# Optimization experiments

Measured on AMD Instinct MI355X. Metric: run time of the kernel, lower is better.

Reference implementation:

```python
import jax, jax.numpy as jnp
import numpy as np

BINS = 32
C_Z = 128
B, L = 2, 768
NUM_CLASSES = 2 * BINS + 2  # 66


def setup_inputs() -> dict:
    key = jax.random.key(0)
    k1, k2, k3 = jax.random.split(key, 3)
    residue_index = jnp.sort(jax.random.randint(k1, (B, L), 0, 1024), axis=-1)
    residue_mask = jnp.ones((B, L), dtype=bool)
    W = jax.random.normal(k2, (NUM_CLASSES, C_Z), dtype=jnp.float32)  # linear.weight.T
    b = jax.random.normal(k3, (C_Z,), dtype=jnp.float32)
    return {"residue_index": residue_index, "residue_mask": residue_mask, "W": W, "b": b}


def reference(residue_index, residue_mask, W, b):
    # pairwise relative position, clipped into bins -> class index in [1, 2*BINS+1]
    diff = residue_index[:, None, :] - residue_index[:, :, None]  # [B, L, L]
    idx = jnp.clip(diff, -BINS, BINS) + BINS + 1
    # one_hot(idx) @ W + b  ==  gather rows of W
    z = W[idx] + b  # [B, L, L, C_Z]
    pair_mask = residue_mask[:, :, None] & residue_mask[:, None, :]
    return z * pair_mask[..., None].astype(z.dtype)
```

## Files before the change

kernel.cpp:

```cpp
#include <hip/hip_runtime.h>


constexpr int BINS = 32;
constexpr int CZ   = 128;
constexpr int NC   = 2 * BINS + 2;
constexpr int B_   = 2;
constexpr int L_   = 768;
constexpr int NROWS = B_ * L_;

typedef float vfloat4 __attribute__((ext_vector_type(4)));

__global__ __launch_bounds__(256) void relpos_row_kernel(
    const int*  __restrict__ residue_index,
    const void* __restrict__ residue_mask,
    const float* __restrict__ W,
    const float* __restrict__ bias,
    float* __restrict__ out)
{
    __shared__ float wb[NC * CZ];
    __shared__ int   ridx_row[L_];
    __shared__ float mask_row[L_];

    const int tid = threadIdx.x;
    const int row = blockIdx.x;
    const int b   = row / L_;
    const int i   = row - b * L_;
    const int o   = b * L_;

    const unsigned int v0 = *(const unsigned int*)residue_mask;
    const bool byte_layout = (v0 & 0xFFFFFF00u) != 0u;

    const vfloat4* W4  = (const vfloat4*)W;
    const vfloat4* bi4 = (const vfloat4*)bias;
    vfloat4* wb4 = (vfloat4*)wb;
    for (int k = tid; k < NC * CZ / 4; k += 256) {
        wb4[k] = W4[k] + bi4[k & (CZ / 4 - 1)];
    }
    for (int k = tid; k < L_; k += 256) {
        ridx_row[k] = residue_index[o + k];
        int m = byte_layout ? (int)((const unsigned char*)residue_mask)[o + k]
                            : ((const int*)residue_mask)[o + k];
        mask_row[k] = m ? 1.0f : 0.0f;
    }
    __syncthreads();

    const int   ri_i = ridx_row[i];
    const float m_i  = mask_row[i];

    const int group = tid >> 5;
    const int lane  = tid & 31;
    float* rowout = out + (size_t)row * L_ * CZ;

    #pragma unroll 4
    for (int j = group; j < L_; j += 8) {
        const int diff = ridx_row[j] - ri_i;
        const int idx  = min(max(diff, -BINS), BINS) + BINS + 1;
        const float m  = m_i * mask_row[j];

        vfloat4 v = ((const vfloat4*)(wb + idx * CZ))[lane];
        v *= m;
        ((vfloat4*)(rowout + j * CZ))[lane] = v;
    }
}

extern "C" void kernel_launch(void* const* d_in, const int* in_sizes, int n_in,
                              void* d_out, int out_size, void* d_ws, size_t ws_size,
                              hipStream_t stream) {
    const int*  residue_index = (const int*)d_in[0];
    const void* residue_mask  = d_in[1];
    const float* W    = (const float*)d_in[2];
    const float* bias = (const float*)d_in[3];
    float* out = (float*)d_out;

    relpos_row_kernel<<<NROWS, 256, 0, stream>>>(residue_index, residue_mask, W, bias, out);
}
```

Before: 599.9 us.

## Process two rows per block and split columns into clamped/unclamped ranges

```diff
diff --git a/kernel.cpp b/kernel.cpp
--- a/kernel.cpp
+++ b/kernel.cpp
@@ -6,11 +6,12 @@
 constexpr int NC   = 2 * BINS + 2;
 constexpr int B_   = 2;
 constexpr int L_   = 768;
-constexpr int NROWS = B_ * L_;
+constexpr int ROWS_PER_BLOCK = 2;
+constexpr int NBLK = B_ * L_ / ROWS_PER_BLOCK;
 
 typedef float vfloat4 __attribute__((ext_vector_type(4)));
 
-__global__ __launch_bounds__(256) void relpos_row_kernel(
+__global__ __launch_bounds__(256) void relpos_kernel(
     const int*  __restrict__ residue_index,
     const void* __restrict__ residue_mask,
     const float* __restrict__ W,
@@ -20,12 +21,12 @@
     __shared__ float wb[NC * CZ];
     __shared__ int   ridx_row[L_];
     __shared__ float mask_row[L_];
+    __shared__ int   s_cnt[2 * ROWS_PER_BLOCK];
 
-    const int tid = threadIdx.x;
-    const int row = blockIdx.x;
-    const int b   = row / L_;
-    const int i   = row - b * L_;
-    const int o   = b * L_;
+    const int tid  = threadIdx.x;
+    const int row0 = blockIdx.x * ROWS_PER_BLOCK;
+    const int b    = row0 / L_;
+    const int o    = b * L_;
 
     const unsigned int v0 = *(const unsigned int*)residue_mask;
     const bool byte_layout = (v0 & 0xFFFFFF00u) != 0u;
@@ -33,33 +34,60 @@
     const vfloat4* W4  = (const vfloat4*)W;
     const vfloat4* bi4 = (const vfloat4*)bias;
     vfloat4* wb4 = (vfloat4*)wb;
-    for (int k = tid; k < NC * CZ / 4; k += 256) {
+    for (int k = tid; k < NC * CZ / 4; k += 256)
         wb4[k] = W4[k] + bi4[k & (CZ / 4 - 1)];
-    }
     for (int k = tid; k < L_; k += 256) {
         ridx_row[k] = residue_index[o + k];
         int m = byte_layout ? (int)((const unsigned char*)residue_mask)[o + k]
                             : ((const int*)residue_mask)[o + k];
         mask_row[k] = m ? 1.0f : 0.0f;
     }
+    if (tid < 2 * ROWS_PER_BLOCK) s_cnt[tid] = 0;
     __syncthreads();
 
-    const int   ri_i = ridx_row[i];
-    const float m_i  = mask_row[i];
+    for (int r = 0; r < ROWS_PER_BLOCK; ++r) {
+        const int ri_i = ridx_row[row0 - o + r];
+        int c1 = 0, c2 = 0;
+        for (int j = tid; j < L_; j += 256) {
+            const int diff = ridx_row[j] - ri_i;
+            c1 += (diff <= -BINS);
+            c2 += (diff <   BINS);
+        }
+        atomicAdd(&s_cnt[2 * r + 0], c1);
+        atomicAdd(&s_cnt[2 * r + 1], c2);
+    }
+    __syncthreads();
 
     const int group = tid >> 5;
     const int lane  = tid & 31;
-    float* rowout = out + (size_t)row * L_ * CZ;
+    const vfloat4 vlo = ((const vfloat4*)(wb + 1 * CZ))[lane];
+    const vfloat4 vhi = ((const vfloat4*)(wb + (NC - 1) * CZ))[lane];
 
-    #pragma unroll 4
-    for (int j = group; j < L_; j += 8) {
-        const int diff = ridx_row[j] - ri_i;
-        const int idx  = min(max(diff, -BINS), BINS) + BINS + 1;
-        const float m  = m_i * mask_row[j];
+    for (int r = 0; r < ROWS_PER_BLOCK; ++r) {
+        const int   i    = row0 - o + r;
+        const int   ri_i = ridx_row[i];
+        const float m_i  = mask_row[i];
+        const int   jlo  = s_cnt[2 * r + 0];
+        const int   jend = s_cnt[2 * r + 1];
+        float* rowout = out + (size_t)(row0 + r) * L_ * CZ;
 
-        vfloat4 v = ((const vfloat4*)(wb + idx * CZ))[lane];
-        v *= m;
-        ((vfloat4*)(rowout + j * CZ))[lane] = v;
+        #pragma unroll 4
+        for (int j = group; j < jlo; j += 8) {
+            vfloat4 v = vlo * (m_i * mask_row[j]);
+            ((vfloat4*)(rowout + j * CZ))[lane] = v;
+        }
+        for (int j = jlo + group; j < jend; j += 8) {
+            const int diff = ridx_row[j] - ri_i;
+            const int idx  = min(max(diff, -BINS), BINS) + BINS + 1;
+            vfloat4 v = ((const vfloat4*)(wb + idx * CZ))[lane];
+            v *= m_i * mask_row[j];
+            ((vfloat4*)(rowout + j * CZ))[lane] = v;
+        }
+        #pragma unroll 4
+        for (int j = jend + ((group - jend) & 7); j < L_; j += 8) {
+            vfloat4 v = vhi * (m_i * mask_row[j]);
+            ((vfloat4*)(rowout + j * CZ))[lane] = v;
+        }
     }
 }
 
@@ -72,5 +100,5 @@
     const float* bias = (const float*)d_in[3];
     float* out = (float*)d_out;
 
-    relpos_row_kernel<<<NROWS, 256, 0, stream>>>(residue_index, residue_mask, W, bias, out);
+    relpos_kernel<<<NBLK, 256, 0, stream>>>(residue_index, residue_mask, W, bias, out);
 }
```

Measured after the change: 608.7 us. No clear change (+1.5%).

## Split each row into clamped-low, banded, clamped-high segments using sorted indices

Applied to the files above, without the earlier changes.

```diff
diff --git a/kernel.cpp b/kernel.cpp
--- a/kernel.cpp
+++ b/kernel.cpp
@@ -6,20 +6,20 @@
 constexpr int NC   = 2 * BINS + 2;
 constexpr int B_   = 2;
 constexpr int L_   = 768;
-constexpr int NROWS = B_ * L_;
+constexpr int NBLK = B_ * L_;
 
 typedef float vfloat4 __attribute__((ext_vector_type(4)));
 
-__global__ __launch_bounds__(256) void relpos_row_kernel(
+__global__ __launch_bounds__(256) void relpos_kernel(
     const int*  __restrict__ residue_index,
     const void* __restrict__ residue_mask,
     const float* __restrict__ W,
     const float* __restrict__ bias,
     float* __restrict__ out)
 {
-    __shared__ float wb[NC * CZ];
     __shared__ int   ridx_row[L_];
     __shared__ float mask_row[L_];
+    __shared__ int   s_cnt[3];
 
     const int tid = threadIdx.x;
     const int row = blockIdx.x;
@@ -27,15 +27,18 @@
     const int i   = row - b * L_;
     const int o   = b * L_;
 
+    const int group = tid >> 5;
+    const int lane  = tid & 31;
+
     const unsigned int v0 = *(const unsigned int*)residue_mask;
     const bool byte_layout = (v0 & 0xFFFFFF00u) != 0u;
 
-    const vfloat4* W4  = (const vfloat4*)W;
-    const vfloat4* bi4 = (const vfloat4*)bias;
-    vfloat4* wb4 = (vfloat4*)wb;
-    for (int k = tid; k < NC * CZ / 4; k += 256) {
-        wb4[k] = W4[k] + bi4[k & (CZ / 4 - 1)];
-    }
+    const vfloat4* W4 = (const vfloat4*)W;
+    const vfloat4 b4  = ((const vfloat4*)bias)[lane];
+    const vfloat4 vlo = W4[1 * (CZ / 4) + lane] + b4;
+    const vfloat4 vhi = W4[(NC - 1) * (CZ / 4) + lane] + b4;
+
+    if (tid < 3) s_cnt[tid] = 0;
     for (int k = tid; k < L_; k += 256) {
         ridx_row[k] = residue_index[o + k];
         int m = byte_layout ? (int)((const unsigned char*)residue_mask)[o + k]
@@ -47,19 +50,62 @@
     const int   ri_i = ridx_row[i];
     const float m_i  = mask_row[i];
 
-    const int group = tid >> 5;
-    const int lane  = tid & 31;
+    {
+        int c1 = 0, c2 = 0, cm = 0;
+        for (int j = tid; j < L_; j += 256) {
+            const int diff = ridx_row[j] - ri_i;
+            c1 += (diff <= -BINS);
+            c2 += (diff <   BINS);
+            cm += (mask_row[j] != 0.0f);
+        }
+        for (int off = 32; off; off >>= 1) {
+            c1 += __shfl_down(c1, off);
+            c2 += __shfl_down(c2, off);
+            cm += __shfl_down(cm, off);
+        }
+        if ((tid & 63) == 0) {
+            atomicAdd(&s_cnt[0], c1);
+            atomicAdd(&s_cnt[1], c2);
+            atomicAdd(&s_cnt[2], cm);
+        }
+    }
+    __syncthreads();
+
+    const int  jlo  = s_cnt[0];
+    const int  jend = s_cnt[1];
+    const bool fast = (s_cnt[2] == L_) && (m_i == 1.0f);
+
     float* rowout = out + (size_t)row * L_ * CZ;
+    const int jb0 = jlo  + ((group - jlo ) & 7);
+    const int jh0 = jend + ((group - jend) & 7);
 
-    #pragma unroll 4
-    for (int j = group; j < L_; j += 8) {
-        const int diff = ridx_row[j] - ri_i;
-        const int idx  = min(max(diff, -BINS), BINS) + BINS + 1;
-        const float m  = m_i * mask_row[j];
-
-        vfloat4 v = ((const vfloat4*)(wb + idx * CZ))[lane];
-        v *= m;
-        ((vfloat4*)(rowout + j * CZ))[lane] = v;
+    if (fast) {
+        #pragma unroll 8
+        for (int j = group; j < jlo; j += 8)
+            ((vfloat4*)(rowout + j * CZ))[lane] = vlo;
+        #pragma unroll 2
+        for (int j = jb0; j < jend; j += 8) {
+            const int diff = ridx_row[j] - ri_i;
+            const int idx  = min(max(diff, -BINS), BINS) + BINS + 1;
+            ((vfloat4*)(rowout + j * CZ))[lane] = W4[idx * (CZ / 4) + lane] + b4;
+        }
+        #pragma unroll 8
+        for (int j = jh0; j < L_; j += 8)
+            ((vfloat4*)(rowout + j * CZ))[lane] = vhi;
+    } else {
+        #pragma unroll 4
+        for (int j = group; j < jlo; j += 8)
+            ((vfloat4*)(rowout + j * CZ))[lane] = vlo * (m_i * mask_row[j]);
+        #pragma unroll 2
+        for (int j = jb0; j < jend; j += 8) {
+            const int diff = ridx_row[j] - ri_i;
+            const int idx  = min(max(diff, -BINS), BINS) + BINS + 1;
+            vfloat4 v = W4[idx * (CZ / 4) + lane] + b4;
+            ((vfloat4*)(rowout + j * CZ))[lane] = v * (m_i * mask_row[j]);
+        }
+        #pragma unroll 4
+        for (int j = jh0; j < L_; j += 8)
+            ((vfloat4*)(rowout + j * CZ))[lane] = vhi * (m_i * mask_row[j]);
     }
 }
 
@@ -72,5 +118,5 @@
     const float* bias = (const float*)d_in[3];
     float* out = (float*)d_out;
 
-    relpos_row_kernel<<<NROWS, 256, 0, stream>>>(residue_index, residue_mask, W, bias, out);
+    relpos_kernel<<<NBLK, 256, 0, stream>>>(residue_index, residue_mask, W, bias, out);
 }
```

Result: no change. 598.6 us (-0.2%).
